# Performance work log

Hardware: AMD Instinct MI355X
Metric: run time of the kernel (lower is better)

The kernel has to match this reference:

```python
import jax, jax.numpy as jnp
import numpy as np

N_NODES = 100000
N_EDGES = 1600000
IN_CH = 128
OUT_CH = 64
NEG_SLOPE = 0.2
EPS = 1e-10


def setup_inputs() -> dict:
    key = jax.random.key(0)
    k1, k2, k3, k4, k5 = jax.random.split(key, 5)
    x = jax.random.normal(k1, (N_NODES, IN_CH), dtype=jnp.float32)
    edge_index = jax.random.randint(k2, (2, N_EDGES), 0, N_NODES, dtype=jnp.int64)
    W = jax.random.normal(k3, (OUT_CH, IN_CH), dtype=jnp.float32) * (1.0 / np.sqrt(IN_CH))
    a_l = jax.random.normal(k4, (OUT_CH,), dtype=jnp.float32) * (1.0 / np.sqrt(OUT_CH))
    a_r = jax.random.normal(k5, (OUT_CH,), dtype=jnp.float32) * (1.0 / np.sqrt(OUT_CH))
    bias = jnp.zeros((OUT_CH,), dtype=jnp.float32)
    return {"x": x, "edge_index": edge_index, "W": W, "a_l": a_l, "a_r": a_r, "bias": bias}


def reference(x, edge_index, W, a_l, a_r, bias):
    N = x.shape[0]
    h = x @ W.T                     # (N, out_ch)
    src, dst = edge_index[0], edge_index[1]
    e_l = h @ a_l                   # (N,)
    e_r = h @ a_r                   # (N,)
    edge_attn = jax.nn.leaky_relu(e_l[dst] + e_r[src], negative_slope=NEG_SLOPE)  # (E,)
    # segment softmax over incoming edges of each dst node
    edge_max = jax.ops.segment_max(edge_attn, dst, num_segments=N)  # (N,), -inf for isolated
    edge_attn = jnp.exp(edge_attn - edge_max[dst])
    edge_sum = jax.ops.segment_sum(edge_attn, dst, num_segments=N)  # (N,)
    edge_attn = edge_attn / (edge_sum[dst] + EPS)
    messages = h[src] * edge_attn[:, None]                          # (E, out_ch)
    out = jax.ops.segment_sum(messages, dst, num_segments=N)        # (N, out_ch)
    return out + bias
```

## Files before the change

### kernel.cpp

```cpp
#include <hip/hip_runtime.h>
#include <math.h>

#define NN 100000
#define NE 1600000
#define IC 128
#define OC 64
#define NEG_SLOPE 0.2f
#define EPS_F 1e-10f

#define NSLICE 200
#define SN 500
#define EB 500
#define QPB 800
#define CAP 12000

typedef short bf16x8 __attribute__((ext_vector_type(8)));
typedef float f32x4 __attribute__((ext_vector_type(4)));

__device__ __forceinline__ unsigned short f2bf(float f) {
    unsigned u = __float_as_uint(f);
    u += 0x7fff + ((u >> 16) & 1);
    return (unsigned short)(u >> 16);
}

__global__ __launch_bounds__(256) void linear_kernel(
    const float* __restrict__ x, const float* __restrict__ W,
    const float* __restrict__ a_l, const float* __restrict__ a_r,
    unsigned short* __restrict__ h_bf, float* __restrict__ e_l,
    float* __restrict__ e_r)
{
    __shared__ unsigned short lds[128 * 136];
    const int tid = threadIdx.x;
    const int n0 = blockIdx.x * 64;

#pragma unroll
    for (int it = 0; it < 8; it++) {
        int i = it * 256 + tid;
        int r = i >> 5, c4 = i & 31;
        int n = n0 + r;
        float4 v = make_float4(0.f, 0.f, 0.f, 0.f);
        if (n < NN) v = *(const float4*)&x[(size_t)n * 128 + (c4 << 2)];
        ushort4 b;
        b.x = f2bf(v.x); b.y = f2bf(v.y); b.z = f2bf(v.z); b.w = f2bf(v.w);
        *(ushort4*)&lds[r * 136 + (c4 << 2)] = b;
    }
#pragma unroll
    for (int it = 0; it < 8; it++) {
        int i = it * 256 + tid;
        int r = i >> 5, c4 = i & 31;
        float4 v = *(const float4*)&W[r * 128 + (c4 << 2)];
        ushort4 b;
        b.x = f2bf(v.x); b.y = f2bf(v.y); b.z = f2bf(v.z); b.w = f2bf(v.w);
        *(ushort4*)&lds[(64 + r) * 136 + (c4 << 2)] = b;
    }
    __syncthreads();

    const int wv = tid >> 6;
    const int lane = tid & 63;
    const int q = lane >> 4;
    const int c = lane & 15;

    f32x4 acc[4];
#pragma unroll
    for (int t = 0; t < 4; t++) acc[t] = (f32x4){0.f, 0.f, 0.f, 0.f};

    const unsigned short* xrow = &lds[(wv * 16 + c) * 136];
    const unsigned short* wrow = &lds[(64 + c) * 136];

#pragma unroll
    for (int kk = 0; kk < 4; kk++) {
        int ko = kk * 32 + q * 8;
        bf16x8 a = *(const bf16x8*)&xrow[ko];
#pragma unroll
        for (int t = 0; t < 4; t++) {
            bf16x8 b = *(const bf16x8*)&wrow[t * 16 * 136 + ko];
            acc[t] = __builtin_amdgcn_mfma_f32_16x16x32_bf16(a, b, acc[t], 0, 0, 0);
        }
    }

#pragma unroll
    for (int r = 0; r < 4; r++) {
        int m = n0 + wv * 16 + q * 4 + r;
        if (m < NN) {
#pragma unroll
            for (int t = 0; t < 4; t++)
                h_bf[(size_t)m * OC + t * 16 + c] = f2bf(acc[t][r]);
        }
    }

    float al[4], ar[4];
#pragma unroll
    for (int t = 0; t < 4; t++) { al[t] = a_l[t * 16 + c]; ar[t] = a_r[t * 16 + c]; }
    float pl[4], pr[4];
#pragma unroll
    for (int r = 0; r < 4; r++) {
        pl[r] = al[0] * acc[0][r] + al[1] * acc[1][r] + al[2] * acc[2][r] + al[3] * acc[3][r];
        pr[r] = ar[0] * acc[0][r] + ar[1] * acc[1][r] + ar[2] * acc[2][r] + ar[3] * acc[3][r];
    }
#pragma unroll
    for (int m = 1; m < 16; m <<= 1) {
#pragma unroll
        for (int r = 0; r < 4; r++) {
            pl[r] += __shfl_xor(pl[r], m);
            pr[r] += __shfl_xor(pr[r], m);
        }
    }
    if (c == 0) {
#pragma unroll
        for (int r = 0; r < 4; r++) {
            int m = n0 + wv * 16 + q * 4 + r;
            if (m < NN) { e_l[m] = pl[r]; e_r[m] = pr[r]; }
        }
    }
}

__global__ __launch_bounds__(256) void hist_kernel(
    const int* __restrict__ dst, int* __restrict__ H)
{
    __shared__ int hist[NSLICE];
    const int t = threadIdx.x, b = blockIdx.x;
    if (t < NSLICE) hist[t] = 0;
    __syncthreads();
    for (int qi = t; qi < QPB; qi += 256) {
        int4 d = ((const int4*)dst)[b * QPB + qi];
        atomicAdd(&hist[d.x / SN], 1);
        atomicAdd(&hist[d.y / SN], 1);
        atomicAdd(&hist[d.z / SN], 1);
        atomicAdd(&hist[d.w / SN], 1);
    }
    __syncthreads();
    if (t < NSLICE) H[t * EB + b] = hist[t];
}

__global__ __launch_bounds__(1024) void scan_block_kernel(
    const int* __restrict__ deg, int* __restrict__ offsets,
    int* __restrict__ bsums)
{
    __shared__ int wsum[16];
    const int t = threadIdx.x;
    const int lane = t & 63, wv = t >> 6;
    const int i = blockIdx.x * 1024 + t;
    int v = (i < NN) ? deg[i] : 0;
    int incl = v;
#pragma unroll
    for (int off = 1; off < 64; off <<= 1) {
        int u = __shfl_up(incl, off);
        if (lane >= off) incl += u;
    }
    if (lane == 63) wsum[wv] = incl;
    __syncthreads();
    if (wv == 0 && lane < 16) {
        int s = wsum[lane];
        int si = s;
#pragma unroll
        for (int off = 1; off < 16; off <<= 1) {
            int u = __shfl_up(si, off);
            if (lane >= off) si += u;
        }
        wsum[lane] = si - s;
    }
    __syncthreads();
    int excl = incl - v + wsum[wv];
    if (i < NN) offsets[i] = excl;
    if (t == 1023) bsums[blockIdx.x] = excl + v;
}

__global__ __launch_bounds__(128) void scan_bsums_kernel(int* __restrict__ bsums)
{
    __shared__ int s[128];
    const int t = threadIdx.x;
    const int NB = (NN + 1023) / 1024;
    int v = (t < NB) ? bsums[t] : 0;
    s[t] = v;
    __syncthreads();
    for (int off = 1; off < 128; off <<= 1) {
        int u = (t >= off) ? s[t - off] : 0;
        __syncthreads();
        s[t] += u;
        __syncthreads();
    }
    if (t < NB) bsums[t] = s[t] - v;
}

__global__ __launch_bounds__(256) void bucket_kernel(
    const int* __restrict__ src, const int* __restrict__ dst,
    const int* __restrict__ O_raw, const int* __restrict__ bsums,
    int* __restrict__ bucketed)
{
    __shared__ int cur[NSLICE];
    const int t = threadIdx.x, b = blockIdx.x;
    if (t < NSLICE) {
        int gi = t * EB + b;
        cur[t] = O_raw[gi] + bsums[gi >> 10];
    }
    __syncthreads();
    for (int qi = t; qi < QPB; qi += 256) {
        int4 d4 = ((const int4*)dst)[b * QPB + qi];
        int4 s4 = ((const int4*)src)[b * QPB + qi];
        int dd[4] = {d4.x, d4.y, d4.z, d4.w};
        int ss[4] = {s4.x, s4.y, s4.z, s4.w};
#pragma unroll
        for (int k = 0; k < 4; k++) {
            int sl = dd[k] / SN;
            int pos = atomicAdd(&cur[sl], 1);
            bucketed[pos] = ((dd[k] - sl * SN) << 17) | ss[k];
        }
    }
}

__global__ __launch_bounds__(1024) void fine_sort_kernel(
    const int* __restrict__ bucketed, const int* __restrict__ O_raw,
    const int* __restrict__ bsums, const float* __restrict__ e_l,
    const float* __restrict__ e_r, float2* __restrict__ sorted_sw,
    int* __restrict__ offsets_out)
{
    __shared__ int ebuf[CAP];
    __shared__ float wbuf[CAP];
    __shared__ int hist[SN];
    __shared__ float nsum[SN];
    __shared__ float el[SN];
    __shared__ int wsums[8];
    const int s = blockIdx.x, t = threadIdx.x;
    int gi0 = s * EB;
    const int B0 = O_raw[gi0] + bsums[gi0 >> 10];
    int B1 = NE;
    if (s < NSLICE - 1) {
        int gi1 = (s + 1) * EB;
        B1 = O_raw[gi1] + bsums[gi1 >> 10];
    }
    int cnt = B1 - B0;
    if (cnt > CAP) cnt = CAP;

    for (int i = t; i < cnt; i += 1024) ebuf[i] = bucketed[B0 + i];
    if (t < SN) {
        hist[t] = 0;
        nsum[t] = 0.f;
        el[t] = e_l[s * SN + t];
    }
    __syncthreads();
    for (int i = t; i < cnt; i += 1024) {
        int p = ebuf[i];
        int dloc = p >> 17;
        int sr = p & 0x1FFFF;
        float a = el[dloc] + e_r[sr];
        a = (a > 0.f) ? a : NEG_SLOPE * a;
        float w = __expf(a);
        wbuf[i] = w;
        atomicAdd(&hist[dloc], 1);
        atomicAdd(&nsum[dloc], w);
    }
    __syncthreads();

    const int lane = t & 63, w8 = t >> 6;
    int v = (t < SN) ? hist[t] : 0;
    int incl = v;
#pragma unroll
    for (int o = 1; o < 64; o <<= 1) {
        int u = __shfl_up(incl, o);
        if (lane >= o) incl += u;
    }
    if (w8 < 8 && lane == 63) wsums[w8] = incl;
    __syncthreads();
    if (t == 0) {
        int run = 0;
#pragma unroll
        for (int k = 0; k < 8; k++) { int x = wsums[k]; wsums[k] = run; run += x; }
    }
    __syncthreads();
    int excl = incl - v + ((w8 < 8) ? wsums[w8] : 0);

    if (t < SN) offsets_out[s * SN + t] = B0 + excl;
    __syncthreads();
    if (t < SN) hist[t] = excl;
    __syncthreads();
    for (int i = t; i < cnt; i += 1024) {
        int p = ebuf[i];
        int dloc = p >> 17;
        int pos = atomicAdd(&hist[dloc], 1);
        float wn = wbuf[i] / (nsum[dloc] + EPS_F);
        sorted_sw[B0 + pos] = make_float2(__int_as_float(p & 0x1FFFF), wn);
    }
    if (s == 0 && t == 0) offsets_out[NN] = NE;
}

__global__ __launch_bounds__(256) void aggregate_kernel(
    const unsigned short* __restrict__ h_bf, const int* __restrict__ offsets,
    const float2* __restrict__ sorted_sw, const float* __restrict__ bias,
    float* __restrict__ out)
{
    const int node = blockIdx.x * 4 + (threadIdx.x >> 6);
    const int lane = threadIdx.x & 63;
    if (node >= NN) return;
    const int start = offsets[node];
    const int end = offsets[node + 1];
    const int grp = lane >> 3;
    const int ch = (lane & 7) * 8;

    float acc[8] = {0.f, 0.f, 0.f, 0.f, 0.f, 0.f, 0.f, 0.f};

#pragma unroll 2
    for (int j = start; j < end; j += 8) {
        int eidx = j + grp;
        int ej = (eidx < end) ? eidx : end - 1;
        float2 p = sorted_sw[ej];
        float w = (eidx < end) ? p.y : 0.f;
        int s = __float_as_int(p.x);
        uint4 qv = *(const uint4*)&h_bf[(size_t)s * OC + ch];
        acc[0] += w * __uint_as_float(qv.x << 16);
        acc[1] += w * __uint_as_float(qv.x & 0xffff0000u);
        acc[2] += w * __uint_as_float(qv.y << 16);
        acc[3] += w * __uint_as_float(qv.y & 0xffff0000u);
        acc[4] += w * __uint_as_float(qv.z << 16);
        acc[5] += w * __uint_as_float(qv.z & 0xffff0000u);
        acc[6] += w * __uint_as_float(qv.w << 16);
        acc[7] += w * __uint_as_float(qv.w & 0xffff0000u);
    }

#pragma unroll
    for (int m = 8; m <= 32; m <<= 1) {
#pragma unroll
        for (int k = 0; k < 8; k++) acc[k] += __shfl_xor(acc[k], m);
    }

    if (lane < 8) {
        float4 b0 = *(const float4*)&bias[lane * 8];
        float4 b1 = *(const float4*)&bias[lane * 8 + 4];
        float4 o0 = make_float4(acc[0] + b0.x, acc[1] + b0.y,
                                acc[2] + b0.z, acc[3] + b0.w);
        float4 o1 = make_float4(acc[4] + b1.x, acc[5] + b1.y,
                                acc[6] + b1.z, acc[7] + b1.w);
        *(float4*)&out[(size_t)node * OC + lane * 8] = o0;
        *(float4*)&out[(size_t)node * OC + lane * 8 + 4] = o1;
    }
}

extern "C" void kernel_launch(void* const* d_in, const int* in_sizes, int n_in,
                              void* d_out, int out_size, void* d_ws, size_t ws_size,
                              hipStream_t stream)
{
    const float* x = (const float*)d_in[0];
    const int* edge_index = (const int*)d_in[1];
    const float* W = (const float*)d_in[2];
    const float* a_l = (const float*)d_in[3];
    const float* a_r = (const float*)d_in[4];
    const float* bias = (const float*)d_in[5];
    float* out = (float*)d_out;

    const int* src = edge_index;
    const int* dst = edge_index + NE;

    char* w = (char*)d_ws;
    unsigned short* h_bf = (unsigned short*)w;
    size_t off = (size_t)NN * OC * 2;
    float* e_l = (float*)(w + off); off += (size_t)NN * 4;
    float* e_r = (float*)(w + off); off += (size_t)NN * 4;
    int* H = (int*)(w + off);       off += (size_t)NN * 4;
    int* O_raw = (int*)(w + off);   off += (size_t)(NN + 4) * 4;
    int* bsums = (int*)(w + off);   off += 128 * 4;
    int* offsets = (int*)(w + off); off += (size_t)(NN + 4) * 4;
    int* bucketed = (int*)(w + off); off += (size_t)NE * 4;
    float2* sorted_sw = (float2*)(w + off); off += (size_t)NE * 8;

    linear_kernel<<<(NN + 63) / 64, 256, 0, stream>>>(x, W, a_l, a_r, h_bf, e_l, e_r);
    hist_kernel<<<EB, 256, 0, stream>>>(dst, H);
    scan_block_kernel<<<(NN + 1023) / 1024, 1024, 0, stream>>>(H, O_raw, bsums);
    scan_bsums_kernel<<<1, 128, 0, stream>>>(bsums);
    bucket_kernel<<<EB, 256, 0, stream>>>(src, dst, O_raw, bsums, bucketed);
    fine_sort_kernel<<<NSLICE, 1024, 0, stream>>>(bucketed, O_raw, bsums, e_l, e_r,
                                                  sorted_sw, offsets);
    aggregate_kernel<<<(NN + 3) / 4, 256, 0, stream>>>(h_bf, offsets, sorted_sw, bias, out);
}
```

Measured before the change: 196.5 us.

## Fuse fine sort with aggregation per slice using LDS-resident sorted edges

Shrinks slices from 500 to 200 destination nodes (500 slices) so each slice's edges fit in LDS, then merges the fine sort and aggregate kernels. Sorted (src, weight) pairs stay in shared memory instead of going through a global sorted_sw array and an offsets array. Softmax normalisation moves to a single per-node multiply after accumulation, and outputs use nontemporal stores. The per-slice capacity drops to 3600 edges, and each block handles 200 nodes with 16 waves, so load balance across blocks and the reduced parallelism of 500 blocks are the tradeoffs.

```diff
diff --git a/kernel.cpp b/kernel.cpp
--- a/kernel.cpp
+++ b/kernel.cpp
@@ -8,11 +8,12 @@
 #define NEG_SLOPE 0.2f
 #define EPS_F 1e-10f
 
-#define NSLICE 200
-#define SN 500
+#define NSLICE 500
+#define SN 200
 #define EB 500
 #define QPB 800
-#define CAP 12000
+#define CAP 3600
+#define SLEN (NSLICE * EB)
 
 typedef short bf16x8 __attribute__((ext_vector_type(8)));
 typedef float f32x4 __attribute__((ext_vector_type(4)));
@@ -119,7 +120,7 @@
 {
     __shared__ int hist[NSLICE];
     const int t = threadIdx.x, b = blockIdx.x;
-    if (t < NSLICE) hist[t] = 0;
+    for (int i = t; i < NSLICE; i += 256) hist[i] = 0;
     __syncthreads();
     for (int qi = t; qi < QPB; qi += 256) {
         int4 d = ((const int4*)dst)[b * QPB + qi];
@@ -129,7 +130,7 @@
         atomicAdd(&hist[d.w / SN], 1);
     }
     __syncthreads();
-    if (t < NSLICE) H[t * EB + b] = hist[t];
+    for (int i = t; i < NSLICE; i += 256) H[i * EB + b] = hist[i];
 }
 
 __global__ __launch_bounds__(1024) void scan_block_kernel(
@@ -140,7 +141,7 @@
     const int t = threadIdx.x;
     const int lane = t & 63, wv = t >> 6;
     const int i = blockIdx.x * 1024 + t;
-    int v = (i < NN) ? deg[i] : 0;
+    int v = (i < SLEN) ? deg[i] : 0;
     int incl = v;
 #pragma unroll
     for (int off = 1; off < 64; off <<= 1) {
@@ -161,19 +162,19 @@
     }
     __syncthreads();
     int excl = incl - v + wsum[wv];
-    if (i < NN) offsets[i] = excl;
+    if (i < SLEN) offsets[i] = excl;
     if (t == 1023) bsums[blockIdx.x] = excl + v;
 }
 
-__global__ __launch_bounds__(128) void scan_bsums_kernel(int* __restrict__ bsums)
-{
-    __shared__ int s[128];
+__global__ __launch_bounds__(256) void scan_bsums_kernel(int* __restrict__ bsums)
+{
+    __shared__ int s[256];
     const int t = threadIdx.x;
-    const int NB = (NN + 1023) / 1024;
+    const int NB = (SLEN + 1023) / 1024;
     int v = (t < NB) ? bsums[t] : 0;
     s[t] = v;
     __syncthreads();
-    for (int off = 1; off < 128; off <<= 1) {
+    for (int off = 1; off < 256; off <<= 1) {
         int u = (t >= off) ? s[t - off] : 0;
         __syncthreads();
         s[t] += u;
@@ -189,9 +190,9 @@
 {
     __shared__ int cur[NSLICE];
     const int t = threadIdx.x, b = blockIdx.x;
-    if (t < NSLICE) {
-        int gi = t * EB + b;
-        cur[t] = O_raw[gi] + bsums[gi >> 10];
+    for (int i = t; i < NSLICE; i += 256) {
+        int gi = i * EB + b;
+        cur[i] = O_raw[gi] + bsums[gi >> 10];
     }
     __syncthreads();
     for (int qi = t; qi < QPB; qi += 256) {
@@ -208,18 +209,18 @@
     }
 }
 
-__global__ __launch_bounds__(1024) void fine_sort_kernel(
+__global__ __launch_bounds__(1024, 8) void fused_sort_agg_kernel(
     const int* __restrict__ bucketed, const int* __restrict__ O_raw,
     const int* __restrict__ bsums, const float* __restrict__ e_l,
-    const float* __restrict__ e_r, float2* __restrict__ sorted_sw,
-    int* __restrict__ offsets_out)
-{
-    __shared__ int ebuf[CAP];
-    __shared__ float wbuf[CAP];
+    const float* __restrict__ e_r, const unsigned short* __restrict__ h_bf,
+    const float* __restrict__ bias, float* __restrict__ out)
+{
+    __shared__ int2 sorted[CAP];
     __shared__ int hist[SN];
     __shared__ float nsum[SN];
     __shared__ float el[SN];
-    __shared__ int wsums[8];
+    __shared__ int wsums[4];
+
     const int s = blockIdx.x, t = threadIdx.x;
     int gi0 = s * EB;
     const int B0 = O_raw[gi0] + bsums[gi0 >> 10];
@@ -231,27 +232,31 @@
     int cnt = B1 - B0;
     if (cnt > CAP) cnt = CAP;
 
-    for (int i = t; i < cnt; i += 1024) ebuf[i] = bucketed[B0 + i];
     if (t < SN) {
         hist[t] = 0;
         nsum[t] = 0.f;
         el[t] = e_l[s * SN + t];
     }
     __syncthreads();
-    for (int i = t; i < cnt; i += 1024) {
-        int p = ebuf[i];
-        int dloc = p >> 17;
-        int sr = p & 0x1FFFF;
-        float a = el[dloc] + e_r[sr];
-        a = (a > 0.f) ? a : NEG_SLOPE * a;
-        float w = __expf(a);
-        wbuf[i] = w;
-        atomicAdd(&hist[dloc], 1);
-        atomicAdd(&nsum[dloc], w);
-    }
-    __syncthreads();
-
-    const int lane = t & 63, w8 = t >> 6;
+
+    int pr[4]; float wr[4];
+#pragma unroll
+    for (int k = 0; k < 4; k++) {
+        int i = t + k * 1024;
+        if (i < cnt) {
+            int p = __builtin_nontemporal_load(&bucketed[B0 + i]);
+            int dloc = p >> 17;
+            float a = el[dloc] + e_r[p & 0x1FFFF];
+            a = (a > 0.f) ? a : NEG_SLOPE * a;
+            float w = __expf(a);
+            pr[k] = p; wr[k] = w;
+            atomicAdd(&hist[dloc], 1);
+            atomicAdd(&nsum[dloc], w);
+        }
+    }
+    __syncthreads();
+
+    const int lane = t & 63, w4 = t >> 6;
     int v = (t < SN) ? hist[t] : 0;
     int incl = v;
 #pragma unroll
@@ -259,78 +264,76 @@
         int u = __shfl_up(incl, o);
         if (lane >= o) incl += u;
     }
-    if (w8 < 8 && lane == 63) wsums[w8] = incl;
+    if (w4 < 4 && lane == 63) wsums[w4] = incl;
     __syncthreads();
     if (t == 0) {
         int run = 0;
 #pragma unroll
-        for (int k = 0; k < 8; k++) { int x = wsums[k]; wsums[k] = run; run += x; }
-    }
-    __syncthreads();
-    int excl = incl - v + ((w8 < 8) ? wsums[w8] : 0);
-
-    if (t < SN) offsets_out[s * SN + t] = B0 + excl;
-    __syncthreads();
+        for (int k = 0; k < 4; k++) { int x = wsums[k]; wsums[k] = run; run += x; }
+    }
+    __syncthreads();
+    int excl = incl - v + ((w4 < 4) ? wsums[w4] : 0);
     if (t < SN) hist[t] = excl;
     __syncthreads();
-    for (int i = t; i < cnt; i += 1024) {
-        int p = ebuf[i];
-        int dloc = p >> 17;
-        int pos = atomicAdd(&hist[dloc], 1);
-        float wn = wbuf[i] / (nsum[dloc] + EPS_F);
-        sorted_sw[B0 + pos] = make_float2(__int_as_float(p & 0x1FFFF), wn);
-    }
-    if (s == 0 && t == 0) offsets_out[NN] = NE;
-}
-
-__global__ __launch_bounds__(256) void aggregate_kernel(
-    const unsigned short* __restrict__ h_bf, const int* __restrict__ offsets,
-    const float2* __restrict__ sorted_sw, const float* __restrict__ bias,
-    float* __restrict__ out)
-{
-    const int node = blockIdx.x * 4 + (threadIdx.x >> 6);
-    const int lane = threadIdx.x & 63;
-    if (node >= NN) return;
-    const int start = offsets[node];
-    const int end = offsets[node + 1];
+
+#pragma unroll
+    for (int k = 0; k < 4; k++) {
+        int i = t + k * 1024;
+        if (i < cnt) {
+            int dloc = pr[k] >> 17;
+            int pos = atomicAdd(&hist[dloc], 1);
+            sorted[pos] = make_int2(pr[k] & 0x1FFFF, __float_as_int(wr[k]));
+        }
+    }
+    __syncthreads();
+
+    const int wv = t >> 6;
     const int grp = lane >> 3;
     const int ch = (lane & 7) * 8;
-
-    float acc[8] = {0.f, 0.f, 0.f, 0.f, 0.f, 0.f, 0.f, 0.f};
+    float4 bb0 = make_float4(0.f, 0.f, 0.f, 0.f), bb1 = bb0;
+    if (lane < 8) {
+        bb0 = *(const float4*)&bias[lane * 8];
+        bb1 = *(const float4*)&bias[lane * 8 + 4];
+    }
+
+    for (int n = wv; n < SN; n += 16) {
+        int start = (n == 0) ? 0 : hist[n - 1];
+        int end = hist[n];
+        float acc[8] = {0.f, 0.f, 0.f, 0.f, 0.f, 0.f, 0.f, 0.f};
 
 #pragma unroll 2
-    for (int j = start; j < end; j += 8) {
-        int eidx = j + grp;
-        int ej = (eidx < end) ? eidx : end - 1;
-        float2 p = sorted_sw[ej];
-        float w = (eidx < end) ? p.y : 0.f;
-        int s = __float_as_int(p.x);
-        uint4 qv = *(const uint4*)&h_bf[(size_t)s * OC + ch];
-        acc[0] += w * __uint_as_float(qv.x << 16);
-        acc[1] += w * __uint_as_float(qv.x & 0xffff0000u);
-        acc[2] += w * __uint_as_float(qv.y << 16);
-        acc[3] += w * __uint_as_float(qv.y & 0xffff0000u);
-        acc[4] += w * __uint_as_float(qv.z << 16);
-        acc[5] += w * __uint_as_float(qv.z & 0xffff0000u);
-        acc[6] += w * __uint_as_float(qv.w << 16);
-        acc[7] += w * __uint_as_float(qv.w & 0xffff0000u);
-    }
-
-#pragma unroll
-    for (int m = 8; m <= 32; m <<= 1) {
-#pragma unroll
-        for (int k = 0; k < 8; k++) acc[k] += __shfl_xor(acc[k], m);
-    }
-
-    if (lane < 8) {
-        float4 b0 = *(const float4*)&bias[lane * 8];
-        float4 b1 = *(const float4*)&bias[lane * 8 + 4];
-        float4 o0 = make_float4(acc[0] + b0.x, acc[1] + b0.y,
-                                acc[2] + b0.z, acc[3] + b0.w);
-        float4 o1 = make_float4(acc[4] + b1.x, acc[5] + b1.y,
-                                acc[6] + b1.z, acc[7] + b1.w);
-        *(float4*)&out[(size_t)node * OC + lane * 8] = o0;
-        *(float4*)&out[(size_t)node * OC + lane * 8 + 4] = o1;
+        for (int j = start; j < end; j += 8) {
+            int eidx = j + grp;
+            int ej = (eidx < end) ? eidx : end - 1;
+            int2 p = sorted[ej];
+            float w = (eidx < end) ? __int_as_float(p.y) : 0.f;
+            uint4 qv = *(const uint4*)&h_bf[(size_t)p.x * OC + ch];
+            acc[0] += w * __uint_as_float(qv.x << 16);
+            acc[1] += w * __uint_as_float(qv.x & 0xffff0000u);
+            acc[2] += w * __uint_as_float(qv.y << 16);
+            acc[3] += w * __uint_as_float(qv.y & 0xffff0000u);
+            acc[4] += w * __uint_as_float(qv.z << 16);
+            acc[5] += w * __uint_as_float(qv.z & 0xffff0000u);
+            acc[6] += w * __uint_as_float(qv.w << 16);
+            acc[7] += w * __uint_as_float(qv.w & 0xffff0000u);
+        }
+
+#pragma unroll
+        for (int m = 8; m <= 32; m <<= 1) {
+#pragma unroll
+            for (int k = 0; k < 8; k++) acc[k] += __shfl_xor(acc[k], m);
+        }
+
+        if (lane < 8) {
+            float rinv = 1.0f / (nsum[n] + EPS_F);
+            int node = s * SN + n;
+            f32x4 o0 = { acc[0] * rinv + bb0.x, acc[1] * rinv + bb0.y,
+                         acc[2] * rinv + bb0.z, acc[3] * rinv + bb0.w };
+            f32x4 o1 = { acc[4] * rinv + bb1.x, acc[5] * rinv + bb1.y,
+                         acc[6] * rinv + bb1.z, acc[7] * rinv + bb1.w };
+            __builtin_nontemporal_store(o0, (f32x4*)&out[(size_t)node * OC + lane * 8]);
+            __builtin_nontemporal_store(o1, (f32x4*)&out[(size_t)node * OC + lane * 8 + 4]);
+        }
     }
 }
 
@@ -354,19 +357,16 @@
     size_t off = (size_t)NN * OC * 2;
     float* e_l = (float*)(w + off); off += (size_t)NN * 4;
     float* e_r = (float*)(w + off); off += (size_t)NN * 4;
-    int* H = (int*)(w + off);       off += (size_t)NN * 4;
-    int* O_raw = (int*)(w + off);   off += (size_t)(NN + 4) * 4;
-    int* bsums = (int*)(w + off);   off += 128 * 4;
-    int* offsets = (int*)(w + off); off += (size_t)(NN + 4) * 4;
+    int* H = (int*)(w + off);       off += (size_t)SLEN * 4;
+    int* O_raw = (int*)(w + off);   off += (size_t)(SLEN + 4) * 4;
+    int* bsums = (int*)(w + off);   off += 256 * 4;
     int* bucketed = (int*)(w + off); off += (size_t)NE * 4;
-    float2* sorted_sw = (float2*)(w + off); off += (size_t)NE * 8;
 
     linear_kernel<<<(NN + 63) / 64, 256, 0, stream>>>(x, W, a_l, a_r, h_bf, e_l, e_r);
     hist_kernel<<<EB, 256, 0, stream>>>(dst, H);
-    scan_block_kernel<<<(NN + 1023) / 1024, 1024, 0, stream>>>(H, O_raw, bsums);
-    scan_bsums_kernel<<<1, 128, 0, stream>>>(bsums);
+    scan_block_kernel<<<(SLEN + 1023) / 1024, 1024, 0, stream>>>(H, O_raw, bsums);
+    scan_bsums_kernel<<<1, 256, 0, stream>>>(bsums);
     bucket_kernel<<<EB, 256, 0, stream>>>(src, dst, O_raw, bsums, bucketed);
-    fine_sort_kernel<<<NSLICE, 1024, 0, stream>>>(bucketed, O_raw, bsums, e_l, e_r,
-                                                  sorted_sw, offsets);
-    aggregate_kernel<<<(NN + 3) / 4, 256, 0, stream>>>(h_bf, offsets, sorted_sw, bias, out);
-}
+    fused_sort_agg_kernel<<<NSLICE, 1024, 0, stream>>>(bucketed, O_raw, bsums, e_l, e_r,
+                                                       h_bf, bias, out);
+}
```

Measured after the change: 190.7 us. -2.9%, faster.
